# Kernel optimization log

Hardware: AMD Instinct MI355X
Metric: run time of the kernel (lower is better)

The kernel has to match this reference:

```python
import jax, jax.numpy as jnp
import numpy as np

B, S, D = 4, 2048, 1024

def setup_inputs() -> dict:
    key = jax.random.key(0)
    ks = jax.random.split(key, 7)
    s = 1.0 / np.sqrt(D)
    return {
        "x":  jax.random.normal(ks[0], (B, S, D), dtype=jnp.float32),
        "Wq": jax.random.uniform(ks[1], (D, D), jnp.float32, -s, s),
        "bq": jax.random.uniform(ks[2], (D,),  jnp.float32, -s, s),
        "Wk": jax.random.uniform(ks[3], (D, D), jnp.float32, -s, s),
        "bk": jax.random.uniform(ks[4], (D,),  jnp.float32, -s, s),
        "Wv": jax.random.uniform(ks[5], (D, D), jnp.float32, -s, s),
        "bv": jax.random.uniform(ks[6], (D,),  jnp.float32, -s, s),
    }

def reference(x, Wq, bq, Wk, bk, Wv, bv):
    # Q/K/V projections: [B,S,D]
    Q = jnp.einsum('bsd,de->bse', x, Wq) + bq
    K = jnp.einsum('bsd,de->bse', x, Wk) + bk
    V = jnp.einsum('bsd,de->bse', x, Wv) + bv
    scale = 1.0 / jnp.sqrt(jnp.asarray(K.shape[-1], K.dtype))
    scores = jnp.einsum('bqd,bkd->bqk', Q, K) * scale  # [B,S,S]
    weights = jax.nn.softmax(scores, axis=-1)
    return jnp.einsum('bqk,bkd->bqd', weights, V)
```

## Files before the change

### kernel.cpp

```cpp
#include <hip/hip_runtime.h>

typedef __attribute__((ext_vector_type(4))) float f32x4;
typedef __attribute__((ext_vector_type(8))) short bf16x8;

__device__ __forceinline__ float bf2f(unsigned short u) {
  union { unsigned int i; float f; } x; x.i = ((unsigned int)u) << 16; return x.f;
}
__device__ __forceinline__ unsigned short f2bf(float f) {
  union { float f; unsigned int i; } x; x.f = f;
  unsigned int r = (x.i + 0x7FFFu + ((x.i >> 16) & 1u)) >> 16;
  return (unsigned short)r;
}

#define BARX __builtin_amdgcn_s_barrier()
#define LGK0 asm volatile("s_waitcnt lgkmcnt(0)" ::: "memory")
#define GLD(gsrc, ldsoff)                                                        \
  __builtin_amdgcn_global_load_lds(                                              \
      (const __attribute__((address_space(1))) void*)(gsrc),                     \
      (__attribute__((address_space(3))) void*)&lds[ldsoff], 16, 0, 0)

__global__ __launch_bounds__(256) void cvt_f2b(const float* __restrict__ src,
                                               unsigned short* __restrict__ dst, long n4) {
  long i = (long)blockIdx.x * 256 + threadIdx.x;
  long stride = (long)gridDim.x * 256;
  for (; i < n4; i += stride) {
    float4 v = *(const float4*)&src[i * 4];
    ushort4 o;
    o.x = f2bf(v.x); o.y = f2bf(v.y); o.z = f2bf(v.z); o.w = f2bf(v.w);
    *(ushort4*)&dst[i * 4] = o;
  }
}

__global__ __launch_bounds__(256) void transpose_f2b(const float* __restrict__ src,
                                                     unsigned short* __restrict__ dst,
                                                     int rows, int cols) {
  __shared__ float t[32][33];
  int bx = blockIdx.x * 32, by = blockIdx.y * 32;
  int tx = threadIdx.x, ty = threadIdx.y;
#pragma unroll
  for (int k = 0; k < 4; ++k)
    t[ty + 8 * k][tx] = src[(long)(by + ty + 8 * k) * cols + bx + tx];
  __syncthreads();
#pragma unroll
  for (int k = 0; k < 4; ++k)
    dst[(long)(bx + ty + 8 * k) * rows + by + tx] = f2bf(t[tx][ty + 8 * k]);
}

__global__ __launch_bounds__(256) void transpose_v(const unsigned short* __restrict__ src,
                                                   unsigned short* __restrict__ dst) {
  __shared__ unsigned short t[32][33];
  const long sb = (long)blockIdx.z * 2048 * 3072;
  const long db = (long)blockIdx.z * 1024 * 2048;
  int bx = blockIdx.x * 32, by = blockIdx.y * 32;
  int tx = threadIdx.x, ty = threadIdx.y;
#pragma unroll
  for (int k = 0; k < 4; ++k)
    t[ty + 8 * k][tx] = src[sb + (long)(by + ty + 8 * k) * 3072 + bx + tx];
  __syncthreads();
#pragma unroll
  for (int k = 0; k < 4; ++k)
    dst[db + (long)(bx + ty + 8 * k) * 2048 + by + tx] = t[tx][ty + 8 * k];
}

template <int MODE>
__global__ __launch_bounds__(512, 2) void gemm2p(const unsigned short* __restrict__ Ap,
                                                 const unsigned short* __restrict__ Bp,
                                                 void* __restrict__ Cv,
                                                 const float* __restrict__ q_,
                                                 const float* __restrict__ k_,
                                                 const float* __restrict__ v_,
                                                 const float* __restrict__ invden,
                                                 int Kd, int lda, int ldb, int ldc, float scale,
                                                 long sA, long sB, long sC) {
  __shared__ unsigned short lds[73728];
  const int bz = blockIdx.z;
  Ap += (long)bz * sA; Bp += (long)bz * sB;
  const int tid = threadIdx.x;
  const int m0 = blockIdx.x * 128, n0 = blockIdx.y * 256;
  const int lane = tid & 63, wave = tid >> 6;
  const int wm = wave >> 2, wn = wave & 3;
  const int rr = tid >> 3;
  const int cSrc = ((tid & 7) ^ (rr & 7)) << 3;
  const int lc = lane & 15, lr = lane >> 4;
  const int x0 = (lc & 4) << 3;
  const int x1 = 32 ^ x0;
  const int klo = (lr << 3) ^ ((lc & 3) << 3);
  const int aoff = (wm * 64 + lc) * 64 + klo;
  const int boff = 8192 + (wn * 64 + lc) * 64 + klo;
  const int NT = Kd >> 6;

  const unsigned short* pA0 = Ap + (long)(m0 + rr) * lda + cSrc;
  const unsigned short* pA1 = pA0 + (long)64 * lda;
  const unsigned short* pB0 = Bp + (long)(n0 + rr) * ldb + cSrc;
  const unsigned short* pB1 = pB0 + (long)64 * ldb;
  const unsigned short* pB2 = pB0 + (long)128 * ldb;
  const unsigned short* pB3 = pB0 + (long)192 * ldb;
  const int dA0 = tid * 8, dA1 = 4096 + tid * 8;
  const int dB0 = 8192 + tid * 8, dB1 = 12288 + tid * 8;
  const int dB2 = 16384 + tid * 8, dB3 = 20480 + tid * 8;
#define STAGE6(so)                                                                \
  { GLD(pB0, (so) + dB0); GLD(pB1, (so) + dB1); GLD(pA0, (so) + dA0);             \
    GLD(pB2, (so) + dB2); GLD(pB3, (so) + dB3); GLD(pA1, (so) + dA1); }
#define ADV { pA0 += 64; pA1 += 64; pB0 += 64; pB1 += 64; pB2 += 64; pB3 += 64; }

  f32x4 acc[4][4] = {};

  STAGE6(0); ADV;
  STAGE6(24576); ADV;
  asm volatile("s_waitcnt vmcnt(6)" ::: "memory");
  BARX;

  int cur = 0;
  for (int t = 0; t < NT; ++t) {
    const int stg = (cur >= 1) ? cur - 1 : 2;
    const unsigned short* Lp = &lds[cur * 24576];
    const int so = stg * 24576;
    const bool pf = (t + 2 < NT);
    bf16x8 a0[2][2], a1[2][2], bb[2][2][2];
#pragma unroll
    for (int nh = 0; nh < 2; ++nh)
#pragma unroll
      for (int ni = 0; ni < 2; ++ni) {
        bb[nh][ni][0] = *(const bf16x8*)&Lp[boff + nh * 2048 + ni * 1024 + x0];
        bb[nh][ni][1] = *(const bf16x8*)&Lp[boff + nh * 2048 + ni * 1024 + x1];
      }
#pragma unroll
    for (int mi = 0; mi < 2; ++mi) {
      a0[mi][0] = *(const bf16x8*)&Lp[aoff + mi * 1024 + x0];
      a0[mi][1] = *(const bf16x8*)&Lp[aoff + mi * 1024 + x1];
    }
    if (pf) { GLD(pB0, so + dB0); GLD(pB1, so + dB1); GLD(pA0, so + dA0); }
    BARX; LGK0;
    __builtin_amdgcn_s_setprio(1);
#pragma unroll
    for (int mi = 0; mi < 2; ++mi)
#pragma unroll
      for (int nh = 0; nh < 2; ++nh)
#pragma unroll
        for (int ni = 0; ni < 2; ++ni)
#pragma unroll
          for (int x = 0; x < 2; ++x)
            acc[mi][nh * 2 + ni] = __builtin_amdgcn_mfma_f32_16x16x32_bf16(
                a0[mi][x], bb[nh][ni][x], acc[mi][nh * 2 + ni], 0, 0, 0);
    __builtin_amdgcn_s_setprio(0);
    BARX;
#pragma unroll
    for (int mi = 0; mi < 2; ++mi) {
      a1[mi][0] = *(const bf16x8*)&Lp[aoff + 2048 + mi * 1024 + x0];
      a1[mi][1] = *(const bf16x8*)&Lp[aoff + 2048 + mi * 1024 + x1];
    }
    if (pf) { GLD(pB2, so + dB2); GLD(pB3, so + dB3); GLD(pA1, so + dA1); }
    BARX; LGK0;
    __builtin_amdgcn_s_setprio(1);
#pragma unroll
    for (int mi = 0; mi < 2; ++mi)
#pragma unroll
      for (int nh = 0; nh < 2; ++nh)
#pragma unroll
        for (int ni = 0; ni < 2; ++ni)
#pragma unroll
          for (int x = 0; x < 2; ++x)
            acc[2 + mi][nh * 2 + ni] = __builtin_amdgcn_mfma_f32_16x16x32_bf16(
                a1[mi][x], bb[nh][ni][x], acc[2 + mi][nh * 2 + ni], 0, 0, 0);
    __builtin_amdgcn_s_setprio(0);
    if (pf) { asm volatile("s_waitcnt vmcnt(6)" ::: "memory"); }
    else    { asm volatile("s_waitcnt vmcnt(0)" ::: "memory"); }
    BARX;
    cur = (cur == 2) ? 0 : cur + 1;
    ADV;
  }
#undef STAGE6
#undef ADV

  const int r0 = m0 + wm * 64 + lr * 4;
  const int c0 = n0 + wn * 64 + lc;
  if (MODE == 2) {
    float* O = (float*)Cv + (long)bz * sC;
    const float* idn = invden + (long)bz * 2048;
#pragma unroll
    for (int j = 0; j < 4; ++j)
#pragma unroll
      for (int r = 0; r < 4; ++r) {
        const int row = r0 + j * 16 + r;
        const float iv = idn[row];
#pragma unroll
        for (int nh = 0; nh < 2; ++nh)
#pragma unroll
          for (int ni = 0; ni < 2; ++ni)
            O[(long)row * ldc + (c0 + nh * 32 + ni * 16)] = acc[j][nh * 2 + ni][r] * iv;
      }
  } else {
    unsigned short* C = (unsigned short*)Cv + (long)bz * sC;
#pragma unroll
    for (int nh = 0; nh < 2; ++nh)
#pragma unroll
      for (int ni = 0; ni < 2; ++ni) {
        const int col = c0 + nh * 32 + ni * 16;
        float bv = 0.0f;
        if (MODE == 0)
          bv = (col < 1024) ? q_[col] : ((col < 2048) ? k_[col - 1024] : v_[col - 2048]);
#pragma unroll
        for (int j = 0; j < 4; ++j)
#pragma unroll
          for (int r = 0; r < 4; ++r) {
            float val = acc[j][nh * 2 + ni][r];
            val = (MODE == 0) ? (val + bv) : __expf(val * scale);
            C[(long)(r0 + j * 16 + r) * ldc + col] = f2bf(val);
          }
      }
  }
}

__global__ __launch_bounds__(256) void rowsum_inv(const unsigned short* __restrict__ E,
                                                  float* __restrict__ invden) {
  const long row = blockIdx.x;
  const unsigned short* p = E + row * 2048;
  const int tid = threadIdx.x;
  const int lane = tid & 63, wave = tid >> 6;
  ushort4 h0 = *(const ushort4*)&p[tid * 8];
  ushort4 h1 = *(const ushort4*)&p[tid * 8 + 4];
  float s = bf2f(h0.x) + bf2f(h0.y) + bf2f(h0.z) + bf2f(h0.w) +
            bf2f(h1.x) + bf2f(h1.y) + bf2f(h1.z) + bf2f(h1.w);
#pragma unroll
  for (int o = 32; o >= 1; o >>= 1) s += __shfl_xor(s, o);
  __shared__ float ss[4];
  if (lane == 0) ss[wave] = s;
  __syncthreads();
  if (tid == 0) invden[row] = 1.0f / (ss[0] + ss[1] + ss[2] + ss[3]);
}

extern "C" void kernel_launch(void* const* d_in, const int* in_sizes, int n_in,
                              void* d_out, int out_size, void* d_ws, size_t ws_size,
                              hipStream_t stream) {
  const float* x  = (const float*)d_in[0];
  const float* Wq = (const float*)d_in[1];
  const float* bq = (const float*)d_in[2];
  const float* Wk = (const float*)d_in[3];
  const float* bk = (const float*)d_in[4];
  const float* Wv = (const float*)d_in[5];
  const float* bv = (const float*)d_in[6];
  float* out = (float*)d_out;

  const int Bb = 4, S = 2048, D = 1024;
  const long MS = (long)Bb * S;

  char* ws = (char*)d_ws;
  unsigned short* xb  = (unsigned short*)(ws);
  unsigned short* Wt  = (unsigned short*)(ws + (16L << 20));
  unsigned short* QKV = (unsigned short*)(ws + (22L << 20));
  unsigned short* Sc  = (unsigned short*)(ws + (70L << 20));
  unsigned short* VT  = xb;
  float* invden = (float*)(ws + (16L << 20));

  cvt_f2b<<<2048, 256, 0, stream>>>(x, xb, MS * D / 4);

  dim3 tb(32, 8);
  dim3 tg(D / 32, D / 32);
  transpose_f2b<<<tg, tb, 0, stream>>>(Wq, Wt, D, D);
  transpose_f2b<<<tg, tb, 0, stream>>>(Wk, Wt + 1024 * 1024, D, D);
  transpose_f2b<<<tg, tb, 0, stream>>>(Wv, Wt + 2 * 1024 * 1024, D, D);

  dim3 pgrid(MS / 128, 3072 / 256, 1);
  gemm2p<0><<<pgrid, 512, 0, stream>>>(xb, Wt, QKV, bq, bk, bv, nullptr,
                                       D, D, D, 3072, 1.0f, 0, 0, 0);

  dim3 vtg(D / 32, S / 32, Bb);
  transpose_v<<<vtg, tb, 0, stream>>>(QKV + 2048, VT);

  dim3 sgrid(S / 128, S / 256, Bb);
  gemm2p<1><<<sgrid, 512, 0, stream>>>(QKV, QKV + 1024, Sc, nullptr, nullptr, nullptr, nullptr,
                                       D, 3072, 3072, S, 1.0f / 32.0f,
                                       (long)S * 3072, (long)S * 3072, (long)S * S);

  rowsum_inv<<<MS, 256, 0, stream>>>(Sc, invden);

  dim3 ogrid(S / 128, D / 256, Bb);
  gemm2p<2><<<ogrid, 512, 0, stream>>>(Sc, VT, out, nullptr, nullptr, nullptr, invden,
                                       S, S, S, D, 1.0f,
                                       (long)S * S, (long)D * S, (long)S * D);
}
```

Measured before the change: 180.6 us.

## Add 256x256-tile ping-pong GEMM for QKV projection and score kernels

Adds a new GEMM kernel using 256x256 output tiles, double-buffered LDS and split A/B half-tile loads interleaved between four MFMA quadrants. It replaces the 128x256 kernel for the QKV projection and the QK^T score/exp stage. The old kernel is kept only for the final PV product. Larger tiles raise arithmetic intensity and cut global loads per FLOP, but they double accumulator registers and halve the number of blocks, which may lower occupancy or leave CUs idle on smaller grids.

```diff
diff --git a/kernel.cpp b/kernel.cpp
--- a/kernel.cpp
+++ b/kernel.cpp
@@ -63,14 +63,148 @@
 }
 
 template <int MODE>
+__global__ __launch_bounds__(512, 2) void gemm8(const unsigned short* __restrict__ Ap,
+                                                const unsigned short* __restrict__ Bp,
+                                                void* __restrict__ Cv,
+                                                const float* __restrict__ q_,
+                                                const float* __restrict__ k_,
+                                                const float* __restrict__ v_,
+                                                int Kd, int lda, int ldb, int ldc, float scale,
+                                                long sA, long sB, long sC) {
+  __shared__ unsigned short lds[65536];
+  const int bz = blockIdx.z;
+  Ap += (long)bz * sA; Bp += (long)bz * sB;
+  const int tid = threadIdx.x;
+  const int m0 = blockIdx.x * 256, n0 = blockIdx.y * 256;
+  const int lane = tid & 63, wave = tid >> 6;
+  const int wm = wave >> 2, wn = wave & 3;
+  const int rr = tid >> 3;
+  const int cSrc = ((tid & 7) ^ (rr & 7)) << 3;
+  const int lc = lane & 15, lr = lane >> 4;
+  const int x0 = (lc & 4) << 3;
+  const int x1 = 32 ^ x0;
+  const int klo = (lr << 3) ^ ((lc & 3) << 3);
+  const int aofs = wm * 4096 + lc * 64 + klo;
+  const int bofs = 16384 + wn * 2048 + lc * 64 + klo;
+  const int NT = Kd >> 6;
+
+#define STA(b, h, kt)                                                                            \
+  {                                                                                              \
+    _Pragma("unroll") for (int i_ = 0; i_ < 2; ++i_) {                                           \
+      const unsigned short* g_ =                                                                 \
+          Ap + (long)(m0 + i_ * 128 + (h) * 64 + rr) * lda + ((kt) * 64 + cSrc);                 \
+      GLD(g_, (b) * 32768 + (h) * 8192 + i_ * 4096 + tid * 8);                                   \
+    }                                                                                            \
+  }
+#define STB(b, h, kt)                                                                            \
+  {                                                                                              \
+    _Pragma("unroll") for (int i_ = 0; i_ < 2; ++i_) {                                           \
+      const unsigned short* g_ =                                                                 \
+          Bp + (long)(n0 + (i_ * 2 + (rr >> 5)) * 64 + (h) * 32 + (rr & 31)) * ldb +             \
+          ((kt) * 64 + cSrc);                                                                    \
+      GLD(g_, (b) * 32768 + 16384 + (h) * 8192 + i_ * 4096 + tid * 8);                           \
+    }                                                                                            \
+  }
+#define MM(mh, nh, A_, B_)                                                                       \
+  _Pragma("unroll") for (int mi = 0; mi < 4; ++mi)                                               \
+      _Pragma("unroll") for (int ni = 0; ni < 2; ++ni)                                           \
+          _Pragma("unroll") for (int x = 0; x < 2; ++x)                                          \
+              acc[(mh) * 4 + mi][(nh) * 2 + ni] = __builtin_amdgcn_mfma_f32_16x16x32_bf16(       \
+                  A_[mi][x], B_[ni][x], acc[(mh) * 4 + mi][(nh) * 2 + ni], 0, 0, 0);
+
+  f32x4 acc[8][4] = {};
+
+  STA(0, 0, 0); STB(0, 0, 0);
+  asm volatile("s_waitcnt vmcnt(4)" ::: "memory");
+  STB(0, 1, 0); STA(0, 1, 0);
+  STA(1, 0, 1); STB(1, 0, 1); STB(1, 1, 1);
+  asm volatile("s_waitcnt vmcnt(6)" ::: "memory");
+  BARX;
+
+  for (int t = 0; t < NT; ++t) {
+    const int p = t & 1, q = p ^ 1;
+    const int Lb = p << 15;
+    bf16x8 a[4][2], b0[2][2], b1[2][2];
+#pragma unroll
+    for (int mi = 0; mi < 4; ++mi) {
+      a[mi][0] = *(const bf16x8*)&lds[Lb + aofs + mi * 1024 + x0];
+      a[mi][1] = *(const bf16x8*)&lds[Lb + aofs + mi * 1024 + x1];
+    }
+#pragma unroll
+    for (int ni = 0; ni < 2; ++ni) {
+      b0[ni][0] = *(const bf16x8*)&lds[Lb + bofs + ni * 1024 + x0];
+      b0[ni][1] = *(const bf16x8*)&lds[Lb + bofs + ni * 1024 + x1];
+    }
+    if (t + 1 < NT) STA(q, 1, t + 1);
+    BARX; LGK0;
+    __builtin_amdgcn_s_setprio(1);
+    MM(0, 0, a, b0);
+    __builtin_amdgcn_s_setprio(0);
+    BARX;
+#pragma unroll
+    for (int ni = 0; ni < 2; ++ni) {
+      b1[ni][0] = *(const bf16x8*)&lds[Lb + bofs + 8192 + ni * 1024 + x0];
+      b1[ni][1] = *(const bf16x8*)&lds[Lb + bofs + 8192 + ni * 1024 + x1];
+    }
+    if (t + 2 < NT) STA(p, 0, t + 2);
+    BARX; LGK0;
+    __builtin_amdgcn_s_setprio(1);
+    MM(0, 1, a, b1);
+    __builtin_amdgcn_s_setprio(0);
+    BARX;
+#pragma unroll
+    for (int mi = 0; mi < 4; ++mi) {
+      a[mi][0] = *(const bf16x8*)&lds[Lb + aofs + 8192 + mi * 1024 + x0];
+      a[mi][1] = *(const bf16x8*)&lds[Lb + aofs + 8192 + mi * 1024 + x1];
+    }
+    if (t + 2 < NT) STB(p, 0, t + 2);
+    BARX; LGK0;
+    __builtin_amdgcn_s_setprio(1);
+    MM(1, 1, a, b1);
+    __builtin_amdgcn_s_setprio(0);
+    BARX;
+    if (t + 2 < NT) STB(p, 1, t + 2);
+    BARX;
+    __builtin_amdgcn_s_setprio(1);
+    MM(1, 0, a, b0);
+    __builtin_amdgcn_s_setprio(0);
+    if (t + 2 < NT) { asm volatile("s_waitcnt vmcnt(6)" ::: "memory"); }
+    else            { asm volatile("s_waitcnt vmcnt(0)" ::: "memory"); }
+    BARX;
+  }
+#undef STA
+#undef STB
+#undef MM
+
+  const int r0 = m0 + wm * 128 + lr * 4;
+  const int c0 = n0 + wn * 64 + lc;
+  unsigned short* C = (unsigned short*)Cv + (long)bz * sC;
+#pragma unroll
+  for (int nh = 0; nh < 2; ++nh)
+#pragma unroll
+    for (int ni = 0; ni < 2; ++ni) {
+      const int col = c0 + nh * 32 + ni * 16;
+      float bv = 0.0f;
+      if (MODE == 0)
+        bv = (col < 1024) ? q_[col] : ((col < 2048) ? k_[col - 1024] : v_[col - 2048]);
+#pragma unroll
+      for (int mh = 0; mh < 2; ++mh)
+#pragma unroll
+        for (int mi = 0; mi < 4; ++mi)
+#pragma unroll
+          for (int r = 0; r < 4; ++r) {
+            float val = acc[mh * 4 + mi][nh * 2 + ni][r];
+            val = (MODE == 0) ? (val + bv) : __expf(val * scale);
+            C[(long)(r0 + mh * 64 + mi * 16 + r) * ldc + col] = f2bf(val);
+          }
+    }
+}
+
 __global__ __launch_bounds__(512, 2) void gemm2p(const unsigned short* __restrict__ Ap,
                                                  const unsigned short* __restrict__ Bp,
-                                                 void* __restrict__ Cv,
-                                                 const float* __restrict__ q_,
-                                                 const float* __restrict__ k_,
-                                                 const float* __restrict__ v_,
+                                                 float* __restrict__ Out,
                                                  const float* __restrict__ invden,
-                                                 int Kd, int lda, int ldb, int ldc, float scale,
+                                                 int Kd, int lda, int ldb, int ldc,
                                                  long sA, long sB, long sC) {
   __shared__ unsigned short lds[73728];
   const int bz = blockIdx.z;
@@ -174,41 +308,20 @@
 
   const int r0 = m0 + wm * 64 + lr * 4;
   const int c0 = n0 + wn * 64 + lc;
-  if (MODE == 2) {
-    float* O = (float*)Cv + (long)bz * sC;
-    const float* idn = invden + (long)bz * 2048;
-#pragma unroll
-    for (int j = 0; j < 4; ++j)
-#pragma unroll
-      for (int r = 0; r < 4; ++r) {
-        const int row = r0 + j * 16 + r;
-        const float iv = idn[row];
-#pragma unroll
-        for (int nh = 0; nh < 2; ++nh)
-#pragma unroll
-          for (int ni = 0; ni < 2; ++ni)
-            O[(long)row * ldc + (c0 + nh * 32 + ni * 16)] = acc[j][nh * 2 + ni][r] * iv;
-      }
-  } else {
-    unsigned short* C = (unsigned short*)Cv + (long)bz * sC;
-#pragma unroll
-    for (int nh = 0; nh < 2; ++nh)
-#pragma unroll
-      for (int ni = 0; ni < 2; ++ni) {
-        const int col = c0 + nh * 32 + ni * 16;
-        float bv = 0.0f;
-        if (MODE == 0)
-          bv = (col < 1024) ? q_[col] : ((col < 2048) ? k_[col - 1024] : v_[col - 2048]);
-#pragma unroll
-        for (int j = 0; j < 4; ++j)
-#pragma unroll
-          for (int r = 0; r < 4; ++r) {
-            float val = acc[j][nh * 2 + ni][r];
-            val = (MODE == 0) ? (val + bv) : __expf(val * scale);
-            C[(long)(r0 + j * 16 + r) * ldc + col] = f2bf(val);
-          }
-      }
-  }
+  float* O = Out + (long)bz * sC;
+  const float* idn = invden + (long)bz * 2048;
+#pragma unroll
+  for (int j = 0; j < 4; ++j)
+#pragma unroll
+    for (int r = 0; r < 4; ++r) {
+      const int row = r0 + j * 16 + r;
+      const float iv = idn[row];
+#pragma unroll
+      for (int nh = 0; nh < 2; ++nh)
+#pragma unroll
+        for (int ni = 0; ni < 2; ++ni)
+          O[(long)row * ldc + (c0 + nh * 32 + ni * 16)] = acc[j][nh * 2 + ni][r] * iv;
+    }
 }
 
 __global__ __launch_bounds__(256) void rowsum_inv(const unsigned short* __restrict__ E,
@@ -260,22 +373,21 @@
   transpose_f2b<<<tg, tb, 0, stream>>>(Wk, Wt + 1024 * 1024, D, D);
   transpose_f2b<<<tg, tb, 0, stream>>>(Wv, Wt + 2 * 1024 * 1024, D, D);
 
-  dim3 pgrid(MS / 128, 3072 / 256, 1);
-  gemm2p<0><<<pgrid, 512, 0, stream>>>(xb, Wt, QKV, bq, bk, bv, nullptr,
-                                       D, D, D, 3072, 1.0f, 0, 0, 0);
+  dim3 pgrid(MS / 256, 3072 / 256, 1);
+  gemm8<0><<<pgrid, 512, 0, stream>>>(xb, Wt, QKV, bq, bk, bv,
+                                      D, D, D, 3072, 1.0f, 0, 0, 0);
 
   dim3 vtg(D / 32, S / 32, Bb);
   transpose_v<<<vtg, tb, 0, stream>>>(QKV + 2048, VT);
 
-  dim3 sgrid(S / 128, S / 256, Bb);
-  gemm2p<1><<<sgrid, 512, 0, stream>>>(QKV, QKV + 1024, Sc, nullptr, nullptr, nullptr, nullptr,
-                                       D, 3072, 3072, S, 1.0f / 32.0f,
-                                       (long)S * 3072, (long)S * 3072, (long)S * S);
+  dim3 sgrid(S / 256, S / 256, Bb);
+  gemm8<1><<<sgrid, 512, 0, stream>>>(QKV, QKV + 1024, Sc, nullptr, nullptr, nullptr,
+                                      D, 3072, 3072, S, 1.0f / 32.0f,
+                                      (long)S * 3072, (long)S * 3072, (long)S * S);
 
   rowsum_inv<<<MS, 256, 0, stream>>>(Sc, invden);
 
   dim3 ogrid(S / 128, D / 256, Bb);
-  gemm2p<2><<<ogrid, 512, 0, stream>>>(Sc, VT, out, nullptr, nullptr, nullptr, invden,
-                                       S, S, S, D, 1.0f,
-                                       (long)S * S, (long)D * S, (long)S * D);
-}
+  gemm2p<<<ogrid, 512, 0, stream>>>(Sc, VT, out, invden, S, S, S, D,
+                                    (long)S * S, (long)D * S, (long)S * D);
+}
```

Measured after the change: 186.5 us. +3.3%, slower.

## Fuse softmax row-sum into PV GEMM, pad leading dims, remap blocks

Applied to the files above, without the earlier changes.

Removes the separate rowsum_inv kernel by accumulating the row sums of the exponentiated scores inside a dedicated P·V GEMM, reading them from the A tiles already staged in LDS. The score and V^T buffers are padded to a leading dimension of 2064 to avoid power-of-two stride conflicts. The new kernel uses a flattened grid with an XCD-aware block remap for cache locality. The V transpose now uses 64x64 tiles. This adds LDS reads and per-tile bf16 converts inside the GEMM main loop, and the padded layout uses more workspace.

```diff
diff --git a/kernel.cpp b/kernel.cpp
--- a/kernel.cpp
+++ b/kernel.cpp
@@ -46,20 +46,21 @@
     dst[(long)(bx + ty + 8 * k) * rows + by + tx] = f2bf(t[tx][ty + 8 * k]);
 }
 
-__global__ __launch_bounds__(256) void transpose_v(const unsigned short* __restrict__ src,
+__global__ __launch_bounds__(512) void transpose_v(const unsigned short* __restrict__ src,
                                                    unsigned short* __restrict__ dst) {
-  __shared__ unsigned short t[32][33];
+  __shared__ unsigned short t[64][65];
   const long sb = (long)blockIdx.z * 2048 * 3072;
-  const long db = (long)blockIdx.z * 1024 * 2048;
-  int bx = blockIdx.x * 32, by = blockIdx.y * 32;
-  int tx = threadIdx.x, ty = threadIdx.y;
-#pragma unroll
-  for (int k = 0; k < 4; ++k)
-    t[ty + 8 * k][tx] = src[sb + (long)(by + ty + 8 * k) * 3072 + bx + tx];
+  const long db = (long)blockIdx.z * 1024 * 2064;
+  const int d0 = blockIdx.x * 64;
+  const int s0 = blockIdx.y * 64;
+  const int tx = threadIdx.x, ty = threadIdx.y;
+#pragma unroll
+  for (int k = 0; k < 8; ++k)
+    t[ty + 8 * k][tx] = src[sb + (long)(s0 + ty + 8 * k) * 3072 + d0 + tx];
   __syncthreads();
 #pragma unroll
-  for (int k = 0; k < 4; ++k)
-    dst[db + (long)(bx + ty + 8 * k) * 2048 + by + tx] = t[tx][ty + 8 * k];
+  for (int k = 0; k < 8; ++k)
+    dst[db + (long)(d0 + ty + 8 * k) * 2064 + s0 + tx] = t[tx][ty + 8 * k];
 }
 
 template <int MODE>
@@ -69,7 +70,6 @@
                                                  const float* __restrict__ q_,
                                                  const float* __restrict__ k_,
                                                  const float* __restrict__ v_,
-                                                 const float* __restrict__ invden,
                                                  int Kd, int lda, int ldb, int ldc, float scale,
                                                  long sA, long sB, long sC) {
   __shared__ unsigned short lds[73728];
@@ -174,59 +174,167 @@
 
   const int r0 = m0 + wm * 64 + lr * 4;
   const int c0 = n0 + wn * 64 + lc;
-  if (MODE == 2) {
-    float* O = (float*)Cv + (long)bz * sC;
-    const float* idn = invden + (long)bz * 2048;
-#pragma unroll
-    for (int j = 0; j < 4; ++j)
-#pragma unroll
-      for (int r = 0; r < 4; ++r) {
-        const int row = r0 + j * 16 + r;
-        const float iv = idn[row];
-#pragma unroll
-        for (int nh = 0; nh < 2; ++nh)
-#pragma unroll
-          for (int ni = 0; ni < 2; ++ni)
-            O[(long)row * ldc + (c0 + nh * 32 + ni * 16)] = acc[j][nh * 2 + ni][r] * iv;
+  unsigned short* C = (unsigned short*)Cv + (long)bz * sC;
+#pragma unroll
+  for (int nh = 0; nh < 2; ++nh)
+#pragma unroll
+    for (int ni = 0; ni < 2; ++ni) {
+      const int col = c0 + nh * 32 + ni * 16;
+      float bv = 0.0f;
+      if (MODE == 0)
+        bv = (col < 1024) ? q_[col] : ((col < 2048) ? k_[col - 1024] : v_[col - 2048]);
+#pragma unroll
+      for (int j = 0; j < 4; ++j)
+#pragma unroll
+        for (int r = 0; r < 4; ++r) {
+          float val = acc[j][nh * 2 + ni][r];
+          val = (MODE == 0) ? (val + bv) : __expf(val * scale);
+          C[(long)(r0 + j * 16 + r) * ldc + col] = f2bf(val);
+        }
+    }
+}
+
+__global__ __launch_bounds__(512, 2) void gemmpv(const unsigned short* __restrict__ Eb,
+                                                 const unsigned short* __restrict__ Vb,
+                                                 float* __restrict__ Out) {
+  __shared__ unsigned short lds[73728];
+  const int LDA = 2064, LDB = 2064, NT = 32;
+  const int flat = blockIdx.x;
+  const int nid = ((flat & 7) << 5) | (flat >> 3);
+  const int bz = nid >> 6;
+  const int yb = (nid >> 4) & 3;
+  const int xb = nid & 15;
+  const unsigned short* Ap = Eb + (long)bz * 2048 * 2064;
+  const unsigned short* Bp = Vb + (long)bz * 1024 * 2064;
+  const int tid = threadIdx.x;
+  const int m0 = xb * 128, n0 = yb * 256;
+  const int lane = tid & 63, wave = tid >> 6;
+  const int wm = wave >> 2, wn = wave & 3;
+  const int rr = tid >> 3;
+  const int cSrc = ((tid & 7) ^ (rr & 7)) << 3;
+  const int lc = lane & 15, lr = lane >> 4;
+  const int x0 = (lc & 4) << 3;
+  const int x1 = 32 ^ x0;
+  const int klo = (lr << 3) ^ ((lc & 3) << 3);
+  const int aoff = (wm * 64 + lc) * 64 + klo;
+  const int boff = 8192 + (wn * 64 + lc) * 64 + klo;
+  const int rS = tid >> 2;
+  const int gS0 = (tid & 3) * 2;
+  const int sAd0 = rS * 64 + ((gS0 ^ (rS & 7)) << 3);
+  const int sAd1 = rS * 64 + (((gS0 + 1) ^ (rS & 7)) << 3);
+
+  const unsigned short* pA0 = Ap + (long)(m0 + rr) * LDA + cSrc;
+  const unsigned short* pA1 = pA0 + (long)64 * LDA;
+  const unsigned short* pB0 = Bp + (long)(n0 + rr) * LDB + cSrc;
+  const unsigned short* pB1 = pB0 + (long)64 * LDB;
+  const unsigned short* pB2 = pB0 + (long)128 * LDB;
+  const unsigned short* pB3 = pB0 + (long)192 * LDB;
+  const int dA0 = tid * 8, dA1 = 4096 + tid * 8;
+  const int dB0 = 8192 + tid * 8, dB1 = 12288 + tid * 8;
+  const int dB2 = 16384 + tid * 8, dB3 = 20480 + tid * 8;
+#define STAGE6(so)                                                                \
+  { GLD(pB0, (so) + dB0); GLD(pB1, (so) + dB1); GLD(pA0, (so) + dA0);             \
+    GLD(pB2, (so) + dB2); GLD(pB3, (so) + dB3); GLD(pA1, (so) + dA1); }
+#define ADV { pA0 += 64; pA1 += 64; pB0 += 64; pB1 += 64; pB2 += 64; pB3 += 64; }
+
+  f32x4 acc[4][4] = {};
+  float esum = 0.0f;
+
+  STAGE6(0); ADV;
+  STAGE6(24576); ADV;
+  asm volatile("s_waitcnt vmcnt(6)" ::: "memory");
+  BARX;
+
+  int cur = 0;
+  for (int t = 0; t < NT; ++t) {
+    const int stg = (cur >= 1) ? cur - 1 : 2;
+    const unsigned short* Lp = &lds[cur * 24576];
+    const int so = stg * 24576;
+    const bool pf = (t + 2 < NT);
+    bf16x8 a0[2][2], a1[2][2], bb[2][2][2];
+#pragma unroll
+    for (int nh = 0; nh < 2; ++nh)
+#pragma unroll
+      for (int ni = 0; ni < 2; ++ni) {
+        bb[nh][ni][0] = *(const bf16x8*)&Lp[boff + nh * 2048 + ni * 1024 + x0];
+        bb[nh][ni][1] = *(const bf16x8*)&Lp[boff + nh * 2048 + ni * 1024 + x1];
       }
-  } else {
-    unsigned short* C = (unsigned short*)Cv + (long)bz * sC;
-#pragma unroll
-    for (int nh = 0; nh < 2; ++nh)
-#pragma unroll
-      for (int ni = 0; ni < 2; ++ni) {
-        const int col = c0 + nh * 32 + ni * 16;
-        float bv = 0.0f;
-        if (MODE == 0)
-          bv = (col < 1024) ? q_[col] : ((col < 2048) ? k_[col - 1024] : v_[col - 2048]);
-#pragma unroll
-        for (int j = 0; j < 4; ++j)
-#pragma unroll
-          for (int r = 0; r < 4; ++r) {
-            float val = acc[j][nh * 2 + ni][r];
-            val = (MODE == 0) ? (val + bv) : __expf(val * scale);
-            C[(long)(r0 + j * 16 + r) * ldc + col] = f2bf(val);
-          }
-      }
+#pragma unroll
+    for (int mi = 0; mi < 2; ++mi) {
+      a0[mi][0] = *(const bf16x8*)&Lp[aoff + mi * 1024 + x0];
+      a0[mi][1] = *(const bf16x8*)&Lp[aoff + mi * 1024 + x1];
+    }
+    if (pf) { GLD(pB0, so + dB0); GLD(pB1, so + dB1); GLD(pA0, so + dA0); }
+    BARX; LGK0;
+    __builtin_amdgcn_s_setprio(1);
+#pragma unroll
+    for (int mi = 0; mi < 2; ++mi)
+#pragma unroll
+      for (int nh = 0; nh < 2; ++nh)
+#pragma unroll
+        for (int ni = 0; ni < 2; ++ni)
+#pragma unroll
+          for (int x = 0; x < 2; ++x)
+            acc[mi][nh * 2 + ni] = __builtin_amdgcn_mfma_f32_16x16x32_bf16(
+                a0[mi][x], bb[nh][ni][x], acc[mi][nh * 2 + ni], 0, 0, 0);
+    __builtin_amdgcn_s_setprio(0);
+    BARX;
+#pragma unroll
+    for (int mi = 0; mi < 2; ++mi) {
+      a1[mi][0] = *(const bf16x8*)&Lp[aoff + 2048 + mi * 1024 + x0];
+      a1[mi][1] = *(const bf16x8*)&Lp[aoff + 2048 + mi * 1024 + x1];
+    }
+    {
+      bf16x8 s0 = *(const bf16x8*)&Lp[sAd0];
+      bf16x8 s1 = *(const bf16x8*)&Lp[sAd1];
+#pragma unroll
+      for (int j = 0; j < 8; ++j)
+        esum += bf2f((unsigned short)s0[j]) + bf2f((unsigned short)s1[j]);
+    }
+    if (pf) { GLD(pB2, so + dB2); GLD(pB3, so + dB3); GLD(pA1, so + dA1); }
+    BARX; LGK0;
+    __builtin_amdgcn_s_setprio(1);
+#pragma unroll
+    for (int mi = 0; mi < 2; ++mi)
+#pragma unroll
+      for (int nh = 0; nh < 2; ++nh)
+#pragma unroll
+        for (int ni = 0; ni < 2; ++ni)
+#pragma unroll
+          for (int x = 0; x < 2; ++x)
+            acc[2 + mi][nh * 2 + ni] = __builtin_amdgcn_mfma_f32_16x16x32_bf16(
+                a1[mi][x], bb[nh][ni][x], acc[2 + mi][nh * 2 + ni], 0, 0, 0);
+    __builtin_amdgcn_s_setprio(0);
+    if (pf) { asm volatile("s_waitcnt vmcnt(6)" ::: "memory"); }
+    else    { asm volatile("s_waitcnt vmcnt(0)" ::: "memory"); }
+    BARX;
+    cur = (cur == 2) ? 0 : cur + 1;
+    ADV;
   }
-}
-
-__global__ __launch_bounds__(256) void rowsum_inv(const unsigned short* __restrict__ E,
-                                                  float* __restrict__ invden) {
-  const long row = blockIdx.x;
-  const unsigned short* p = E + row * 2048;
-  const int tid = threadIdx.x;
-  const int lane = tid & 63, wave = tid >> 6;
-  ushort4 h0 = *(const ushort4*)&p[tid * 8];
-  ushort4 h1 = *(const ushort4*)&p[tid * 8 + 4];
-  float s = bf2f(h0.x) + bf2f(h0.y) + bf2f(h0.z) + bf2f(h0.w) +
-            bf2f(h1.x) + bf2f(h1.y) + bf2f(h1.z) + bf2f(h1.w);
-#pragma unroll
-  for (int o = 32; o >= 1; o >>= 1) s += __shfl_xor(s, o);
-  __shared__ float ss[4];
-  if (lane == 0) ss[wave] = s;
+#undef STAGE6
+#undef ADV
+
+  esum += __shfl_xor(esum, 1);
+  esum += __shfl_xor(esum, 2);
+  float* sums = (float*)lds;
+  if ((tid & 3) == 0) sums[tid >> 2] = esum;
   __syncthreads();
-  if (tid == 0) invden[row] = 1.0f / (ss[0] + ss[1] + ss[2] + ss[3]);
+
+  const int r0 = m0 + wm * 64 + lr * 4;
+  const int c0 = n0 + wn * 64 + lc;
+  float* O = Out + (long)bz * (2048L * 1024);
+#pragma unroll
+  for (int j = 0; j < 4; ++j)
+#pragma unroll
+    for (int r = 0; r < 4; ++r) {
+      const int row = r0 + j * 16 + r;
+      const float iv = 1.0f / sums[wm * 64 + lr * 4 + j * 16 + r];
+#pragma unroll
+      for (int nh = 0; nh < 2; ++nh)
+#pragma unroll
+        for (int ni = 0; ni < 2; ++ni)
+          O[(long)row * 1024 + (c0 + nh * 32 + ni * 16)] = acc[j][nh * 2 + ni][r] * iv;
+    }
 }
 
 extern "C" void kernel_launch(void* const* d_in, const int* in_sizes, int n_in,
@@ -243,6 +351,7 @@
 
   const int Bb = 4, S = 2048, D = 1024;
   const long MS = (long)Bb * S;
+  const int LDP = 2064;
 
   char* ws = (char*)d_ws;
   unsigned short* xb  = (unsigned short*)(ws);
@@ -250,7 +359,6 @@
   unsigned short* QKV = (unsigned short*)(ws + (22L << 20));
   unsigned short* Sc  = (unsigned short*)(ws + (70L << 20));
   unsigned short* VT  = xb;
-  float* invden = (float*)(ws + (16L << 20));
 
   cvt_f2b<<<2048, 256, 0, stream>>>(x, xb, MS * D / 4);
 
@@ -261,21 +369,17 @@
   transpose_f2b<<<tg, tb, 0, stream>>>(Wv, Wt + 2 * 1024 * 1024, D, D);
 
   dim3 pgrid(MS / 128, 3072 / 256, 1);
-  gemm2p<0><<<pgrid, 512, 0, stream>>>(xb, Wt, QKV, bq, bk, bv, nullptr,
+  gemm2p<0><<<pgrid, 512, 0, stream>>>(xb, Wt, QKV, bq, bk, bv,
                                        D, D, D, 3072, 1.0f, 0, 0, 0);
 
-  dim3 vtg(D / 32, S / 32, Bb);
-  transpose_v<<<vtg, tb, 0, stream>>>(QKV + 2048, VT);
+  dim3 vtb(64, 8);
+  dim3 vtg(D / 64, S / 64, Bb);
+  transpose_v<<<vtg, vtb, 0, stream>>>(QKV + 2048, VT);
 
   dim3 sgrid(S / 128, S / 256, Bb);
-  gemm2p<1><<<sgrid, 512, 0, stream>>>(QKV, QKV + 1024, Sc, nullptr, nullptr, nullptr, nullptr,
-                                       D, 3072, 3072, S, 1.0f / 32.0f,
-                                       (long)S * 3072, (long)S * 3072, (long)S * S);
-
-  rowsum_inv<<<MS, 256, 0, stream>>>(Sc, invden);
-
-  dim3 ogrid(S / 128, D / 256, Bb);
-  gemm2p<2><<<ogrid, 512, 0, stream>>>(Sc, VT, out, nullptr, nullptr, nullptr, invden,
-                                       S, S, S, D, 1.0f,
-                                       (long)S * S, (long)D * S, (long)S * D);
-}
+  gemm2p<1><<<sgrid, 512, 0, stream>>>(QKV, QKV + 1024, Sc, nullptr, nullptr, nullptr,
+                                       D, 3072, 3072, LDP, 1.0f / 32.0f,
+                                       (long)S * 3072, (long)S * 3072, (long)S * LDP);
+
+  gemmpv<<<256, 512, 0, stream>>>(Sc, VT, out);
+}
```

After: 174.4 us. 3.4% less time.
